# Optimization experiments

Hardware: AMD Instinct MI355X
Metric: run time of the kernel (lower is better)

## Reference

```python
import jax, jax.numpy as jnp
import numpy as np

FEAT_STRIDE = 16
SCORE_THRESH = 0.7
DIST_THRESH = 16.0
MAX_OUT = 50
B = 2048
IMG_W = 65536


def setup_inputs() -> dict:
    key = jax.random.key(0)
    k1, k2, k3 = jax.random.split(key, 3)
    fw = IMG_W // FEAT_STRIDE
    pred_cls_logit = jax.random.normal(k1, (B, fw), dtype=jnp.float32)
    pred_delta = jax.random.normal(k2, (B, fw, 2), dtype=jnp.float32)
    # realistic image widths in [0.5, 1.0] * img_width
    real_images_width = jax.random.uniform(k3, (B,), jnp.float32, 0.5, 1.0) * IMG_W
    return {
        "pred_cls_logit": pred_cls_logit,
        "pred_delta": pred_delta,
        "img_width": IMG_W,
        "real_images_width": real_images_width,
    }


def _nms_one(positions, scores):
    # positions: [N, 2], scores: [N]. Greedy 1D NMS, fixed MAX_OUT iterations.
    centers = positions.mean(axis=1)                      # [N]
    alive0 = scores >= SCORE_THRESH                       # score-threshold filter

    def step(alive, _):
        masked = jnp.where(alive, scores, -1e30)
        i = jnp.argmax(masked)                            # highest remaining score
        has = jnp.any(alive)
        f = has.astype(jnp.float32)                       # 1.0 if a box was picked
        p = positions[i] * f
        s = scores[i] * f
        # suppress everything within DIST_THRESH of picked center (incl. itself)
        new_alive = alive & (jnp.abs(centers - centers[i]) > DIST_THRESH)
        return new_alive, (p, s, f)

    _, (P, S, F) = jax.lax.scan(step, alive0, None, length=MAX_OUT)
    # pad_to_fixed_size: append validity flag column, zero-padded rows
    nms_positions = jnp.concatenate([P, F[:, None]], axis=1)   # [MAX_OUT, 3]
    nms_scores = jnp.concatenate([S[:, None], F[:, None]], axis=1)  # [MAX_OUT, 2]
    return nms_positions, nms_scores


def reference(pred_cls_logit, pred_delta, img_width, real_images_width):
    feat_width = img_width // FEAT_STRIDE
    interval_center = (jnp.arange(feat_width, dtype=jnp.float32) + 0.5) * FEAT_STRIDE
    # [B, feat_width, 2]
    pos = pred_delta * FEAT_STRIDE + interval_center[None, :, None]
    scores = jax.nn.sigmoid(pred_cls_logit)               # [B, feat_width]
    max_width = real_images_width[:, None, None] - 1.0
    pos = jnp.where(pos < 0.0, 0.0, pos)
    pos = jnp.where(pos > max_width, max_width, pos)

    nms_positions, nms_scores = jax.vmap(_nms_one)(pos, scores)

    nms_center = nms_positions[..., :2].mean(axis=2)      # [B, MAX_OUT]
    x_interval_num = jnp.floor(nms_center / FEAT_STRIDE).astype(jnp.int32)
    valid = nms_positions[..., 2] == 1.0
    idx = jnp.where(valid, x_interval_num, feat_width)    # out-of-range -> dropped
    cls_ids = jax.vmap(
        lambda ii: jnp.zeros((feat_width,), jnp.float32).at[ii].set(1.0, mode='drop')
    )(idx)                                                # [B, feat_width]
    return nms_positions, nms_scores, cls_ids
```

## Files before the change

kernel.cpp:

```cpp
#include <hip/hip_runtime.h>
#include <math.h>

#define FW 4096
#define MAX_OUT 50
#define WCAP 320
#define NSLOT 1024
#define T0 0.885f
#define SELCAP 128


__global__ __launch_bounds__(256) void essp_k1(
    const float* __restrict__ logits,
    const float* __restrict__ deltas,
    const float* __restrict__ realw,
    float* stage)
{
  __shared__ float Lx[4][WCAP];
  __shared__ int   Li[4][WCAP];
  __shared__ int   Lcnt[4];
  __shared__ int   Lsel, Lalv;

  const int row  = blockIdx.x;
  const int tid  = threadIdx.x;
  const int lane = tid & 63;
  const int w    = tid >> 6;

  if (tid == 0) { Lsel = 0; Lalv = 0; }

  const float mw = realw[row] - 1.0f;
  const float* lgr = logits + (size_t)row * FW;
  const float* dlr = deltas + (size_t)row * (2 * FW);
  const unsigned long long below = (1ULL << lane) - 1ULL;

  int cnt = 0;
  #pragma unroll
  for (int r = 0; r < 4; ++r) {
    const int i0 = w * 1024 + r * 256 + 4 * lane;
    const float4 lx = *(const float4*)(lgr + i0);
    const float xs[4] = {lx.x, lx.y, lx.z, lx.w};
    bool c4[4]; unsigned long long m4[4];
    #pragma unroll
    for (int e = 0; e < 4; ++e) { c4[e] = (xs[e] >= 0.846f); m4[e] = __ballot(c4[e]); }
    int base = cnt + __popcll(m4[0] & below) + __popcll(m4[1] & below)
                   + __popcll(m4[2] & below) + __popcll(m4[3] & below);
    int off = 0;
    #pragma unroll
    for (int e = 0; e < 4; ++e) {
      if (c4[e]) {
        const int slot = base + off;
        if (slot < WCAP) { Lx[w][slot] = xs[e]; Li[w][slot] = i0 + e; }
        ++off;
      }
    }
    cnt += __popcll(m4[0]) + __popcll(m4[1]) + __popcll(m4[2]) + __popcll(m4[3]);
  }
  if (lane == 0) Lcnt[w] = (cnt < WCAP) ? cnt : WCAP;
  __syncthreads();

  const int c0 = Lcnt[0], c1 = Lcnt[1], c2 = Lcnt[2], c3 = Lcnt[3];
  const int p1 = c0, p2 = c0 + c1, p3 = c0 + c1 + c2;
  int nc = p3 + c3; nc = (nc < NSLOT) ? nc : NSLOT;

  float* Srow = stage + (size_t)row * FW;
  unsigned short* idxrow = (unsigned short*)(Srow + 2048);
  unsigned long long* keyrow = (unsigned long long*)(Srow + 2560);

  #pragma unroll
  for (int g0 = 0; g0 < NSLOT; g0 += 256) {
    const int g = g0 + tid;
    float score = -1e30f, cen = 0.0f;
    int idx = 0;
    if (g < nc) {
      const int wsel = (g >= p1) + (g >= p2) + (g >= p3);
      int pre = 0;
      pre = (wsel == 1) ? p1 : pre;
      pre = (wsel == 2) ? p2 : pre;
      pre = (wsel == 3) ? p3 : pre;
      const int kk = g - pre;
      const float x = (&Lx[0][0])[wsel * WCAP + kk];
      idx = (&Li[0][0])[wsel * WCAP + kk];
      const float2 d = *(const float2*)(dlr + 2 * idx);
      const float ic = ((float)idx + 0.5f) * 16.0f;
      float q0 = d.x * 16.0f + ic;
      float q1 = d.y * 16.0f + ic;
      q0 = (q0 < 0.f) ? 0.f : q0;  q0 = (q0 > mw) ? mw : q0;
      q1 = (q1 < 0.f) ? 0.f : q1;  q1 = (q1 > mw) ? mw : q1;
      cen = (q0 + q1) * 0.5f;
      const float s = (float)(1.0 / (1.0 + exp(-(double)x)));
      score = (s >= 0.7f) ? s : -1e30f;
    }
    Srow[g]        = score;
    Srow[1024 + g] = cen;
    idxrow[g]      = (unsigned short)idx;

    const unsigned long long am = __ballot(score >= 0.7f);
    if (lane == 0) atomicAdd(&Lalv, __popcll(am));
    const unsigned long long sm = __ballot(score >= T0);
    int sbase = 0;
    if (lane == 0 && sm) sbase = atomicAdd(&Lsel, __popcll(sm));
    sbase = __shfl(sbase, 0, 64);
    if (score >= T0) {
      const int pos = sbase + __popcll(sm & below);
      if (pos < SELCAP) {
        keyrow[pos] = (((unsigned long long)__float_as_uint(score)) << 11)
                      | (unsigned)(2047 - g);
        Srow[2816 + pos] = cen;
      }
    }
  }
  __syncthreads();
  if (tid == 0) {
    *(int*)(Srow + 2944) = Lsel;
    *(int*)(Srow + 2945) = Lalv;
  }
}

#define KDEF(J, SS, CE)                                                       \
  const unsigned kb##J = ((SS) >= 0.7f) ? __float_as_uint(SS) : 0u;           \
  const float c##J = (CE);

#define INIT1F(J, SLOTEXPR)                                                   \
  unsigned long long fk##J = kb##J                                            \
      ? ((((unsigned long long)kb##J) << 11) | (unsigned)(2047 - (SLOTEXPR))) \
      : 0ULL;

#define M2(RK, RC, KA, CA, KB, CB)                                            \
  const bool t##RK = (KB) > (KA);                                             \
  const unsigned long long RK = t##RK ? (KB) : (KA);                          \
  const float RC = t##RK ? (CB) : (CA);

#define BSTEP(CTRL) {                                                         \
  const unsigned lo_ = (unsigned)__builtin_amdgcn_update_dpp(                 \
      (int)(unsigned)bk, (int)(unsigned)bk, CTRL, 0xF, 0xF, false);           \
  const unsigned hi_ = (unsigned)__builtin_amdgcn_update_dpp(                 \
      (int)(unsigned)(bk >> 32), (int)(unsigned)(bk >> 32), CTRL, 0xF, 0xF,   \
      false);                                                                 \
  const float oc_ = __int_as_float(__builtin_amdgcn_update_dpp(               \
      __float_as_int(bc), __float_as_int(bc), CTRL, 0xF, 0xF, false));        \
  const unsigned long long ok_ = ((unsigned long long)hi_ << 32) | lo_;       \
  const bool tb_ = ok_ > bk;                                                  \
  bk = tb_ ? ok_ : bk;  bc = tb_ ? oc_ : bc; }

#define SUPF(J) {                                                             \
  const bool ts_ = fabsf(c##J - wc) <= 16.0f;                                 \
  fk##J = ts_ ? 0ULL : fk##J; }

__global__ __launch_bounds__(64) void essp_k2(
    const float* __restrict__ deltas,
    const float* __restrict__ realw,
    float* out_pos,
    float* out_scr,
    float* cls_all)
{
  const int row  = blockIdx.x;
  const int lane = threadIdx.x;
  const int l4   = 4 * lane;
  float* Srow = cls_all + (size_t)row * FW;

  const int sel = *(const int*)(Srow + 2944);
  const int alv = *(const int*)(Srow + 2945);

  int pkv = -1;
  float psv = 0.f;
  bool need_heavy = (sel > SELCAP);

  if (!need_heavy) {
    const unsigned long long* kp = (const unsigned long long*)(Srow + 2560);
    unsigned long long ka = (lane < sel)      ? kp[lane]      : 0ULL;
    unsigned long long kb = (lane + 64 < sel) ? kp[lane + 64] : 0ULL;
    const float ca = (lane < sel)      ? Srow[2816 + lane]      : 0.f;
    const float cb = (lane + 64 < sel) ? Srow[2816 + 64 + lane] : 0.f;

    int cacc = 0;
    #pragma unroll 1
    for (int it = 0; it < MAX_OUT; ++it) {
      const bool tm = kb > ka;
      unsigned long long bk = tm ? kb : ka;
      float bc = tm ? cb : ca;
      BSTEP(0xB1)
      BSTEP(0x4E)
      BSTEP(0x141)
      BSTEP(0x140)
      BSTEP(0x142)
      BSTEP(0x143)
      const unsigned rhi = (unsigned)__builtin_amdgcn_readlane(
          (int)(unsigned)(bk >> 32), 63);
      const unsigned rlo = (unsigned)__builtin_amdgcn_readlane(
          (int)(unsigned)bk, 63);
      const float rc = __int_as_float(
          __builtin_amdgcn_readlane(__float_as_int(bc), 63));
      const unsigned sbits = (rhi << 21) | (rlo >> 11);
      if (sbits == 0u) break;
      if (lane == it) {
        pkv = 2047 - (int)(rlo & 0x7FFu);
        psv = __uint_as_float(sbits);
      }
      ++cacc;
      const float wc = rc;
      if (fabsf(ca - wc) <= 16.0f) ka = 0ULL;
      if (fabsf(cb - wc) <= 16.0f) kb = 0ULL;
    }
    if (cacc < MAX_OUT && alv > sel) { need_heavy = true; pkv = -1; psv = 0.f; }
  }

  if (need_heavy) {
    const float4 s4a = *(const float4*)(Srow + l4);
    const float4 s4b = *(const float4*)(Srow + 256 + l4);
    const float4 s4c = *(const float4*)(Srow + 512 + l4);
    const float4 s4d = *(const float4*)(Srow + 768 + l4);
    const float4 e4a = *(const float4*)(Srow + 1024 + l4);
    const float4 e4b = *(const float4*)(Srow + 1280 + l4);
    const float4 e4c = *(const float4*)(Srow + 1536 + l4);
    const float4 e4d = *(const float4*)(Srow + 1792 + l4);

    KDEF(0,  s4a.x, e4a.x)  KDEF(1,  s4a.y, e4a.y)
    KDEF(2,  s4a.z, e4a.z)  KDEF(3,  s4a.w, e4a.w)
    KDEF(4,  s4b.x, e4b.x)  KDEF(5,  s4b.y, e4b.y)
    KDEF(6,  s4b.z, e4b.z)  KDEF(7,  s4b.w, e4b.w)
    KDEF(8,  s4c.x, e4c.x)  KDEF(9,  s4c.y, e4c.y)
    KDEF(10, s4c.z, e4c.z)  KDEF(11, s4c.w, e4c.w)
    KDEF(12, s4d.x, e4d.x)  KDEF(13, s4d.y, e4d.y)
    KDEF(14, s4d.z, e4d.z)  KDEF(15, s4d.w, e4d.w)

    INIT1F(0,  l4 + 0)       INIT1F(1,  l4 + 1)       INIT1F(2,  l4 + 2)
    INIT1F(3,  l4 + 3)       INIT1F(4,  256 + l4 + 0) INIT1F(5,  256 + l4 + 1)
    INIT1F(6,  256 + l4 + 2) INIT1F(7,  256 + l4 + 3) INIT1F(8,  512 + l4 + 0)
    INIT1F(9,  512 + l4 + 1) INIT1F(10, 512 + l4 + 2) INIT1F(11, 512 + l4 + 3)
    INIT1F(12, 768 + l4 + 0) INIT1F(13, 768 + l4 + 1) INIT1F(14, 768 + l4 + 2)
    INIT1F(15, 768 + l4 + 3)

    #pragma unroll 1
    for (int it = 0; it < MAX_OUT; ++it) {
      M2(ka0, ca0, fk0,  c0,  fk1,  c1)
      M2(ka1, ca1, fk2,  c2,  fk3,  c3)
      M2(ka2, ca2, fk4,  c4,  fk5,  c5)
      M2(ka3, ca3, fk6,  c6,  fk7,  c7)
      M2(ka4, ca4, fk8,  c8,  fk9,  c9)
      M2(ka5, ca5, fk10, c10, fk11, c11)
      M2(ka6, ca6, fk12, c12, fk13, c13)
      M2(ka7, ca7, fk14, c14, fk15, c15)
      M2(kb0, cb0, ka0, ca0, ka1, ca1)
      M2(kb1, cb1, ka2, ca2, ka3, ca3)
      M2(kb2, cb2, ka4, ca4, ka5, ca5)
      M2(kb3, cb3, ka6, ca6, ka7, ca7)
      M2(kc0, cc0, kb0, cb0, kb1, cb1)
      M2(kc1, cc1, kb2, cb2, kb3, cb3)
      M2(kd0, cd0, kc0, cc0, kc1, cc1)

      unsigned long long bk = kd0;
      float bc = cd0;
      BSTEP(0xB1) BSTEP(0x4E) BSTEP(0x141) BSTEP(0x140) BSTEP(0x142) BSTEP(0x143)

      const unsigned rhi = (unsigned)__builtin_amdgcn_readlane(
          (int)(unsigned)(bk >> 32), 63);
      const unsigned rlo = (unsigned)__builtin_amdgcn_readlane(
          (int)(unsigned)bk, 63);
      const float rc = __int_as_float(
          __builtin_amdgcn_readlane(__float_as_int(bc), 63));
      const unsigned sbits = (rhi << 21) | (rlo >> 11);
      const bool valid = sbits != 0u;
      const float wc = valid ? rc : 3.0e38f;
      if (lane == it) {
        pkv = valid ? (2047 - (int)(rlo & 0x7FFu)) : -1;
        psv = __uint_as_float(sbits);
      }
      SUPF(0)  SUPF(1)  SUPF(2)  SUPF(3)  SUPF(4)  SUPF(5)  SUPF(6)  SUPF(7)
      SUPF(8)  SUPF(9)  SUPF(10) SUPF(11) SUPF(12) SUPF(13) SUPF(14) SUPF(15)
    }
  }

  float p0 = 0.f, p1 = 0.f;
  int ci = -1;
  if (pkv >= 0) {
    const int idx = ((const unsigned short*)(Srow + 2048))[pkv];
    const float2 d = *(const float2*)(deltas + (size_t)row * (2 * FW) + 2 * idx);
    const float mw = realw[row] - 1.0f;
    const float ic = ((float)idx + 0.5f) * 16.0f;
    p0 = d.x * 16.0f + ic;
    p1 = d.y * 16.0f + ic;
    p0 = (p0 < 0.f) ? 0.f : p0;  p0 = (p0 > mw) ? mw : p0;
    p1 = (p1 < 0.f) ? 0.f : p1;  p1 = (p1 > mw) ? mw : p1;
    ci = (int)floorf(((p0 + p1) * 0.5f) * 0.0625f);
  }
  asm volatile("s_waitcnt vmcnt(0)" ::: "memory");

  const float4 z4 = make_float4(0.f, 0.f, 0.f, 0.f);
  #pragma unroll
  for (int q = 0; q < 16; ++q)
    *(float4*)(Srow + 256 * q + l4) = z4;
  asm volatile("s_waitcnt vmcnt(0)" ::: "memory");

  float* prow = out_pos + (size_t)row * (MAX_OUT * 3);
  float* srow = out_scr + (size_t)row * (MAX_OUT * 2);
  if (lane < MAX_OUT) {
    if (pkv >= 0) {
      prow[3 * lane + 0] = p0;
      prow[3 * lane + 1] = p1;
      prow[3 * lane + 2] = 1.0f;
      srow[2 * lane + 0] = psv;
      srow[2 * lane + 1] = 1.0f;
      if (ci >= 0 && ci < FW) Srow[ci] = 1.0f;
    } else {
      prow[3 * lane + 0] = 0.0f;
      prow[3 * lane + 1] = 0.0f;
      prow[3 * lane + 2] = 0.0f;
      srow[2 * lane + 0] = 0.0f;
      srow[2 * lane + 1] = 0.0f;
    }
  }
}

extern "C" void kernel_launch(void* const* d_in, const int* in_sizes, int n_in,
                              void* d_out, int out_size, void* d_ws, size_t ws_size,
                              hipStream_t stream) {
  const float* logits = (const float*)d_in[0];
  const float* deltas = (const float*)d_in[1];
  const float* realw  = (const float*)d_in[3];
  const int Bn = in_sizes[3];
  float* out_pos = (float*)d_out;
  float* out_scr = out_pos + (size_t)Bn * MAX_OUT * 3;
  float* out_cls = out_scr + (size_t)Bn * MAX_OUT * 2;

  essp_k1<<<Bn, 256, 0, stream>>>(logits, deltas, realw, out_cls);
  essp_k2<<<Bn, 64, 0, stream>>>(deltas, realw, out_pos, out_scr, out_cls);
}
```

Measured before the change: 77.23 us.

## Sort candidate keys with wave bitonic network and run linear greedy NMS scan

The fast path now packs each candidate into a 32-bit key: the score offset from the threshold bit pattern, combined with the slot index. A wavefront bitonic sort over two keys per lane replaces the 50 iterations of max-reduction. A single in-order pass then picks boxes whose centers are not within range of any already-picked center, using a ballot against the picked centers held one per lane. The heavy fallback moves into a noinline function to ease register pressure on the fast path. The sequential scan can run up to sel iterations, and the sort adds fixed overhead.

```diff
diff --git a/kernel.cpp b/kernel.cpp
--- a/kernel.cpp
+++ b/kernel.cpp
@@ -6,6 +6,7 @@
 #define WCAP 320
 #define NSLOT 1024
 #define T0 0.885f
+#define T0BITS 0x3F628F5Cu
 #define SELCAP 128
 
 
@@ -63,7 +64,7 @@
 
   float* Srow = stage + (size_t)row * FW;
   unsigned short* idxrow = (unsigned short*)(Srow + 2048);
-  unsigned long long* keyrow = (unsigned long long*)(Srow + 2560);
+  unsigned* keyrow = (unsigned*)(Srow + 2560);
 
   #pragma unroll
   for (int g0 = 0; g0 < NSLOT; g0 += 256) {
@@ -102,9 +103,9 @@
     if (score >= T0) {
       const int pos = sbase + __popcll(sm & below);
       if (pos < SELCAP) {
-        keyrow[pos] = (((unsigned long long)__float_as_uint(score)) << 11)
-                      | (unsigned)(2047 - g);
-        Srow[2816 + pos] = cen;
+        keyrow[pos] = ((__float_as_uint(score) - T0BITS + 1u) << 10)
+                      | (unsigned)(1023 - g);
+        Srow[2688 + pos] = cen;
       }
     }
   }
@@ -145,6 +146,117 @@
   const bool ts_ = fabsf(c##J - wc) <= 16.0f;                                 \
   fk##J = ts_ ? 0ULL : fk##J; }
 
+struct PR { int pkv; float psv; };
+
+__device__ __attribute__((noinline)) PR heavy_nms(const float* Srow, int lane) {
+  const int l4 = 4 * lane;
+  const float4 s4a = *(const float4*)(Srow + l4);
+  const float4 s4b = *(const float4*)(Srow + 256 + l4);
+  const float4 s4c = *(const float4*)(Srow + 512 + l4);
+  const float4 s4d = *(const float4*)(Srow + 768 + l4);
+  const float4 e4a = *(const float4*)(Srow + 1024 + l4);
+  const float4 e4b = *(const float4*)(Srow + 1280 + l4);
+  const float4 e4c = *(const float4*)(Srow + 1536 + l4);
+  const float4 e4d = *(const float4*)(Srow + 1792 + l4);
+
+  KDEF(0,  s4a.x, e4a.x)  KDEF(1,  s4a.y, e4a.y)
+  KDEF(2,  s4a.z, e4a.z)  KDEF(3,  s4a.w, e4a.w)
+  KDEF(4,  s4b.x, e4b.x)  KDEF(5,  s4b.y, e4b.y)
+  KDEF(6,  s4b.z, e4b.z)  KDEF(7,  s4b.w, e4b.w)
+  KDEF(8,  s4c.x, e4c.x)  KDEF(9,  s4c.y, e4c.y)
+  KDEF(10, s4c.z, e4c.z)  KDEF(11, s4c.w, e4c.w)
+  KDEF(12, s4d.x, e4d.x)  KDEF(13, s4d.y, e4d.y)
+  KDEF(14, s4d.z, e4d.z)  KDEF(15, s4d.w, e4d.w)
+
+  INIT1F(0,  l4 + 0)       INIT1F(1,  l4 + 1)       INIT1F(2,  l4 + 2)
+  INIT1F(3,  l4 + 3)       INIT1F(4,  256 + l4 + 0) INIT1F(5,  256 + l4 + 1)
+  INIT1F(6,  256 + l4 + 2) INIT1F(7,  256 + l4 + 3) INIT1F(8,  512 + l4 + 0)
+  INIT1F(9,  512 + l4 + 1) INIT1F(10, 512 + l4 + 2) INIT1F(11, 512 + l4 + 3)
+  INIT1F(12, 768 + l4 + 0) INIT1F(13, 768 + l4 + 1) INIT1F(14, 768 + l4 + 2)
+  INIT1F(15, 768 + l4 + 3)
+
+  int pkv = -1; float psv = 0.f;
+  #pragma unroll 1
+  for (int it = 0; it < MAX_OUT; ++it) {
+    M2(ka0, ca0, fk0,  c0,  fk1,  c1)
+    M2(ka1, ca1, fk2,  c2,  fk3,  c3)
+    M2(ka2, ca2, fk4,  c4,  fk5,  c5)
+    M2(ka3, ca3, fk6,  c6,  fk7,  c7)
+    M2(ka4, ca4, fk8,  c8,  fk9,  c9)
+    M2(ka5, ca5, fk10, c10, fk11, c11)
+    M2(ka6, ca6, fk12, c12, fk13, c13)
+    M2(ka7, ca7, fk14, c14, fk15, c15)
+    M2(kb0, cb0, ka0, ca0, ka1, ca1)
+    M2(kb1, cb1, ka2, ca2, ka3, ca3)
+    M2(kb2, cb2, ka4, ca4, ka5, ca5)
+    M2(kb3, cb3, ka6, ca6, ka7, ca7)
+    M2(kc0, cc0, kb0, cb0, kb1, cb1)
+    M2(kc1, cc1, kb2, cb2, kb3, cb3)
+    M2(kd0, cd0, kc0, cc0, kc1, cc1)
+
+    unsigned long long bk = kd0;
+    float bc = cd0;
+    BSTEP(0xB1) BSTEP(0x4E) BSTEP(0x141) BSTEP(0x140) BSTEP(0x142) BSTEP(0x143)
+
+    const unsigned rhi = (unsigned)__builtin_amdgcn_readlane(
+        (int)(unsigned)(bk >> 32), 63);
+    const unsigned rlo = (unsigned)__builtin_amdgcn_readlane(
+        (int)(unsigned)bk, 63);
+    const float rc = __int_as_float(
+        __builtin_amdgcn_readlane(__float_as_int(bc), 63));
+    const unsigned sbits = (rhi << 21) | (rlo >> 11);
+    const bool valid = sbits != 0u;
+    const float wc = valid ? rc : 3.0e38f;
+    if (lane == it) {
+      pkv = valid ? (2047 - (int)(rlo & 0x7FFu)) : -1;
+      psv = __uint_as_float(sbits);
+    }
+    SUPF(0)  SUPF(1)  SUPF(2)  SUPF(3)  SUPF(4)  SUPF(5)  SUPF(6)  SUPF(7)
+    SUPF(8)  SUPF(9)  SUPF(10) SUPF(11) SUPF(12) SUPF(13) SUPF(14) SUPF(15)
+  }
+  PR r; r.pkv = pkv; r.psv = psv; return r;
+}
+
+#define SHX1(v)  (unsigned)__builtin_amdgcn_update_dpp((int)(v), (int)(v), 0xB1, 0xF, 0xF, false)
+#define SHX2(v)  (unsigned)__builtin_amdgcn_update_dpp((int)(v), (int)(v), 0x4E, 0xF, 0xF, false)
+#define SHX4(v)  (unsigned)__builtin_amdgcn_ds_swizzle((int)(v), 0x101F)
+#define SHX8(v)  (unsigned)__builtin_amdgcn_ds_swizzle((int)(v), 0x201F)
+#define SHX16(v) (unsigned)__builtin_amdgcn_ds_swizzle((int)(v), 0x401F)
+#define SHX32(v) (unsigned)__shfl_xor((int)(v), 32, 64)
+
+#define CEX(SH, J, K) {                                                       \
+  const unsigned pk0_ = SH(k0), pk1_ = SH(k1);                                \
+  const unsigned pc0_ = SH(c0), pc1_ = SH(c1);                                \
+  const bool a_  = (lane & (J)) != 0;                                         \
+  const bool b0_ = ((K) <= 32) ? ((lane & (K)) != 0) : false;                 \
+  const bool b1_ = ((K) <= 32) ? ((lane & (K)) != 0) : ((K) == 64);           \
+  const bool x0_ = (a_ != b0_);                                               \
+  const bool x1_ = (a_ != b1_);                                               \
+  {                                                                           \
+    const bool g_ = (k0 > pk0_);                                              \
+    const unsigned mx_ = g_ ? k0 : pk0_;                                      \
+    const unsigned mn_ = g_ ? pk0_ : k0;                                      \
+    const unsigned kn_ = x0_ ? mn_ : mx_;                                     \
+    c0 = (kn_ != k0) ? pc0_ : c0;                                             \
+    k0 = kn_;                                                                 \
+  }                                                                           \
+  {                                                                           \
+    const bool g_ = (k1 > pk1_);                                              \
+    const unsigned mx_ = g_ ? k1 : pk1_;                                      \
+    const unsigned mn_ = g_ ? pk1_ : k1;                                      \
+    const unsigned kn_ = x1_ ? mn_ : mx_;                                     \
+    c1 = (kn_ != k1) ? pc1_ : c1;                                             \
+    k1 = kn_;                                                                 \
+  }                                                                           \
+}
+
+#define CEXP() {                                                              \
+  const bool sw_ = (k1 > k0);                                                 \
+  const unsigned tk_ = k0, tc_ = c0;                                          \
+  k0 = sw_ ? k1 : k0;  c0 = sw_ ? c1 : c0;                                    \
+  k1 = sw_ ? tk_ : k1; c1 = sw_ ? tc_ : c1;                                   \
+}
+
 __global__ __launch_bounds__(64) void essp_k2(
     const float* __restrict__ deltas,
     const float* __restrict__ realw,
@@ -165,122 +277,66 @@
   bool need_heavy = (sel > SELCAP);
 
   if (!need_heavy) {
-    const unsigned long long* kp = (const unsigned long long*)(Srow + 2560);
-    unsigned long long ka = (lane < sel)      ? kp[lane]      : 0ULL;
-    unsigned long long kb = (lane + 64 < sel) ? kp[lane + 64] : 0ULL;
-    const float ca = (lane < sel)      ? Srow[2816 + lane]      : 0.f;
-    const float cb = (lane + 64 < sel) ? Srow[2816 + 64 + lane] : 0.f;
-
-    int cacc = 0;
+    const unsigned* kp = (const unsigned*)(Srow + 2560);
+    unsigned k0 = (lane < sel)      ? kp[lane]      : 0u;
+    unsigned k1 = (lane + 64 < sel) ? kp[lane + 64] : 0u;
+    unsigned c0 = (lane < sel)
+        ? __float_as_uint(Srow[2688 + lane]) : 0u;
+    unsigned c1 = (lane + 64 < sel)
+        ? __float_as_uint(Srow[2688 + 64 + lane]) : 0u;
+
+    CEX(SHX1, 1, 2)
+    CEX(SHX2, 2, 4)   CEX(SHX1, 1, 4)
+    CEX(SHX4, 4, 8)   CEX(SHX2, 2, 8)   CEX(SHX1, 1, 8)
+    CEX(SHX8, 8, 16)  CEX(SHX4, 4, 16)  CEX(SHX2, 2, 16)  CEX(SHX1, 1, 16)
+    CEX(SHX16, 16, 32) CEX(SHX8, 8, 32) CEX(SHX4, 4, 32)  CEX(SHX2, 2, 32)
+    CEX(SHX1, 1, 32)
+    CEX(SHX32, 32, 64) CEX(SHX16, 16, 64) CEX(SHX8, 8, 64) CEX(SHX4, 4, 64)
+    CEX(SHX2, 2, 64)  CEX(SHX1, 1, 64)
+    CEXP()
+    CEX(SHX32, 32, 128) CEX(SHX16, 16, 128) CEX(SHX8, 8, 128)
+    CEX(SHX4, 4, 128)  CEX(SHX2, 2, 128)   CEX(SHX1, 1, 128)
+
+    int npick = 0;
+    float pcen = 3.0e33f;
+    unsigned pkey = 0u;
     #pragma unroll 1
-    for (int it = 0; it < MAX_OUT; ++it) {
-      const bool tm = kb > ka;
-      unsigned long long bk = tm ? kb : ka;
-      float bc = tm ? cb : ca;
-      BSTEP(0xB1)
-      BSTEP(0x4E)
-      BSTEP(0x141)
-      BSTEP(0x140)
-      BSTEP(0x142)
-      BSTEP(0x143)
-      const unsigned rhi = (unsigned)__builtin_amdgcn_readlane(
-          (int)(unsigned)(bk >> 32), 63);
-      const unsigned rlo = (unsigned)__builtin_amdgcn_readlane(
-          (int)(unsigned)bk, 63);
-      const float rc = __int_as_float(
-          __builtin_amdgcn_readlane(__float_as_int(bc), 63));
-      const unsigned sbits = (rhi << 21) | (rlo >> 11);
-      if (sbits == 0u) break;
-      if (lane == it) {
-        pkv = 2047 - (int)(rlo & 0x7FFu);
-        psv = __uint_as_float(sbits);
+    for (int i = 0; i < sel && npick < MAX_OUT; ++i) {
+      const unsigned kiv = (unsigned)__builtin_amdgcn_readlane(
+          (int)(i < 64 ? k0 : k1), i & 63);
+      const float civ = __uint_as_float((unsigned)__builtin_amdgcn_readlane(
+          (int)(i < 64 ? c0 : c1), i & 63));
+      const unsigned long long hm = __ballot(fabsf(pcen - civ) <= 16.0f);
+      if (hm == 0ULL) {
+        if (lane == npick) { pcen = civ; pkey = kiv; }
+        ++npick;
       }
-      ++cacc;
-      const float wc = rc;
-      if (fabsf(ca - wc) <= 16.0f) ka = 0ULL;
-      if (fabsf(cb - wc) <= 16.0f) kb = 0ULL;
-    }
-    if (cacc < MAX_OUT && alv > sel) { need_heavy = true; pkv = -1; psv = 0.f; }
+    }
+    if (npick < MAX_OUT && alv > sel) {
+      need_heavy = true;
+    } else if (lane < npick) {
+      pkv = 1023 - (int)(pkey & 1023u);
+      psv = __uint_as_float(((pkey >> 10) - 1u) + T0BITS);
+    }
   }
 
   if (need_heavy) {
-    const float4 s4a = *(const float4*)(Srow + l4);
-    const float4 s4b = *(const float4*)(Srow + 256 + l4);
-    const float4 s4c = *(const float4*)(Srow + 512 + l4);
-    const float4 s4d = *(const float4*)(Srow + 768 + l4);
-    const float4 e4a = *(const float4*)(Srow + 1024 + l4);
-    const float4 e4b = *(const float4*)(Srow + 1280 + l4);
-    const float4 e4c = *(const float4*)(Srow + 1536 + l4);
-    const float4 e4d = *(const float4*)(Srow + 1792 + l4);
-
-    KDEF(0,  s4a.x, e4a.x)  KDEF(1,  s4a.y, e4a.y)
-    KDEF(2,  s4a.z, e4a.z)  KDEF(3,  s4a.w, e4a.w)
-    KDEF(4,  s4b.x, e4b.x)  KDEF(5,  s4b.y, e4b.y)
-    KDEF(6,  s4b.z, e4b.z)  KDEF(7,  s4b.w, e4b.w)
-    KDEF(8,  s4c.x, e4c.x)  KDEF(9,  s4c.y, e4c.y)
-    KDEF(10, s4c.z, e4c.z)  KDEF(11, s4c.w, e4c.w)
-    KDEF(12, s4d.x, e4d.x)  KDEF(13, s4d.y, e4d.y)
-    KDEF(14, s4d.z, e4d.z)  KDEF(15, s4d.w, e4d.w)
-
-    INIT1F(0,  l4 + 0)       INIT1F(1,  l4 + 1)       INIT1F(2,  l4 + 2)
-    INIT1F(3,  l4 + 3)       INIT1F(4,  256 + l4 + 0) INIT1F(5,  256 + l4 + 1)
-    INIT1F(6,  256 + l4 + 2) INIT1F(7,  256 + l4 + 3) INIT1F(8,  512 + l4 + 0)
-    INIT1F(9,  512 + l4 + 1) INIT1F(10, 512 + l4 + 2) INIT1F(11, 512 + l4 + 3)
-    INIT1F(12, 768 + l4 + 0) INIT1F(13, 768 + l4 + 1) INIT1F(14, 768 + l4 + 2)
-    INIT1F(15, 768 + l4 + 3)
-
-    #pragma unroll 1
-    for (int it = 0; it < MAX_OUT; ++it) {
-      M2(ka0, ca0, fk0,  c0,  fk1,  c1)
-      M2(ka1, ca1, fk2,  c2,  fk3,  c3)
-      M2(ka2, ca2, fk4,  c4,  fk5,  c5)
-      M2(ka3, ca3, fk6,  c6,  fk7,  c7)
-      M2(ka4, ca4, fk8,  c8,  fk9,  c9)
-      M2(ka5, ca5, fk10, c10, fk11, c11)
-      M2(ka6, ca6, fk12, c12, fk13, c13)
-      M2(ka7, ca7, fk14, c14, fk15, c15)
-      M2(kb0, cb0, ka0, ca0, ka1, ca1)
-      M2(kb1, cb1, ka2, ca2, ka3, ca3)
-      M2(kb2, cb2, ka4, ca4, ka5, ca5)
-      M2(kb3, cb3, ka6, ca6, ka7, ca7)
-      M2(kc0, cc0, kb0, cb0, kb1, cb1)
-      M2(kc1, cc1, kb2, cb2, kb3, cb3)
-      M2(kd0, cd0, kc0, cc0, kc1, cc1)
-
-      unsigned long long bk = kd0;
-      float bc = cd0;
-      BSTEP(0xB1) BSTEP(0x4E) BSTEP(0x141) BSTEP(0x140) BSTEP(0x142) BSTEP(0x143)
-
-      const unsigned rhi = (unsigned)__builtin_amdgcn_readlane(
-          (int)(unsigned)(bk >> 32), 63);
-      const unsigned rlo = (unsigned)__builtin_amdgcn_readlane(
-          (int)(unsigned)bk, 63);
-      const float rc = __int_as_float(
-          __builtin_amdgcn_readlane(__float_as_int(bc), 63));
-      const unsigned sbits = (rhi << 21) | (rlo >> 11);
-      const bool valid = sbits != 0u;
-      const float wc = valid ? rc : 3.0e38f;
-      if (lane == it) {
-        pkv = valid ? (2047 - (int)(rlo & 0x7FFu)) : -1;
-        psv = __uint_as_float(sbits);
-      }
-      SUPF(0)  SUPF(1)  SUPF(2)  SUPF(3)  SUPF(4)  SUPF(5)  SUPF(6)  SUPF(7)
-      SUPF(8)  SUPF(9)  SUPF(10) SUPF(11) SUPF(12) SUPF(13) SUPF(14) SUPF(15)
-    }
-  }
-
-  float p0 = 0.f, p1 = 0.f;
+    const PR pr = heavy_nms(Srow, lane);
+    pkv = pr.pkv; psv = pr.psv;
+  }
+
+  float q0 = 0.f, q1 = 0.f;
   int ci = -1;
-  if (pkv >= 0) {
+  if (lane < MAX_OUT && pkv >= 0) {
     const int idx = ((const unsigned short*)(Srow + 2048))[pkv];
     const float2 d = *(const float2*)(deltas + (size_t)row * (2 * FW) + 2 * idx);
     const float mw = realw[row] - 1.0f;
     const float ic = ((float)idx + 0.5f) * 16.0f;
-    p0 = d.x * 16.0f + ic;
-    p1 = d.y * 16.0f + ic;
-    p0 = (p0 < 0.f) ? 0.f : p0;  p0 = (p0 > mw) ? mw : p0;
-    p1 = (p1 < 0.f) ? 0.f : p1;  p1 = (p1 > mw) ? mw : p1;
-    ci = (int)floorf(((p0 + p1) * 0.5f) * 0.0625f);
+    q0 = d.x * 16.0f + ic;
+    q1 = d.y * 16.0f + ic;
+    q0 = (q0 < 0.f) ? 0.f : q0;  q0 = (q0 > mw) ? mw : q0;
+    q1 = (q1 < 0.f) ? 0.f : q1;  q1 = (q1 > mw) ? mw : q1;
+    ci = (int)floorf(((q0 + q1) * 0.5f) * 0.0625f);
   }
   asm volatile("s_waitcnt vmcnt(0)" ::: "memory");
 
@@ -294,8 +350,8 @@
   float* srow = out_scr + (size_t)row * (MAX_OUT * 2);
   if (lane < MAX_OUT) {
     if (pkv >= 0) {
-      prow[3 * lane + 0] = p0;
-      prow[3 * lane + 1] = p1;
+      prow[3 * lane + 0] = q0;
+      prow[3 * lane + 1] = q1;
       prow[3 * lane + 2] = 1.0f;
       srow[2 * lane + 0] = psv;
       srow[2 * lane + 1] = 1.0f;
```

New measurement: 71.52 us. -7.4%, faster.
